# Optimization experiments

Measured on AMD Instinct MI355X. Metric: run time of the kernel, lower is better.

## Reference

```python
import jax, jax.numpy as jnp
from jax import lax
import numpy as np

NPOINT = 1024
NSAMPLE = 32
BN_EPS = 1e-3  # Keras BatchNormalization default epsilon


def farthest_point_sample(xyz, npoint):
    # xyz: [B, N, 3] -> indices [B, npoint] (int32), sequential O(npoint*N)
    B, N, _ = xyz.shape

    def step(carry, _):
        distance, farthest = carry                                   # [B,N], [B]
        centroid = jnp.take_along_axis(xyz, farthest[:, None, None], axis=1)  # [B,1,3]
        dist = jnp.sum((xyz - centroid) ** 2, axis=-1)               # [B,N]
        distance = jnp.minimum(distance, dist)
        new_farthest = jnp.argmax(distance, axis=1).astype(jnp.int32)
        return (distance, new_farthest), farthest

    init = (jnp.full((B, N), 1e10, xyz.dtype), jnp.zeros((B,), jnp.int32))
    _, idxs = lax.scan(step, init, xs=None, length=npoint)           # [npoint, B]
    return jnp.transpose(idxs)                                       # [B, npoint]


def index_points_2d(points, idx):
    # points: [B,N,C], idx: [B,S] -> [B,S,C]
    return jnp.take_along_axis(points, idx[:, :, None], axis=1)


def index_points_3d(points, idx):
    # points: [B,N,C], idx: [B,S,K] -> [B,S,K,C]
    return jax.vmap(lambda p, i: p[i])(points, idx)


def query_ball_point(nsample, xyz, new_xyz):
    # nearest-nsample variant (radius is ignored, matching the source)
    # sq_dist: [B, S, N]
    sq = jnp.sum(new_xyz ** 2, axis=-1, keepdims=True) \
         - 2.0 * jnp.einsum('bsc,bnc->bsn', new_xyz, xyz) \
         + jnp.sum(xyz ** 2, axis=-1)[:, None, :]
    _, group_idx = lax.top_k(-sq, nsample)                           # [B,S,K]
    return group_idx


def bn_relu(x, g, b, mm, mv):
    # inference-mode BatchNorm (moving stats) + ReLU, per-channel on last dim
    return jax.nn.relu((x - mm) * lax.rsqrt(mv + BN_EPS) * g + b)


def setup_inputs() -> dict:
    key = jax.random.key(0)
    ks = jax.random.split(key, 20)
    B, N, D = 4, 16384, 64
    mlp = [64, 64, 128]
    cin = 3 + D  # 67
    inp = {
        'xyz': jax.random.normal(ks[0], (B, N, 3), jnp.float32),
        'points': jax.random.normal(ks[1], (B, N, D), jnp.float32),
    }
    c = cin
    for i, co in enumerate(mlp):
        inp[f'w{i}'] = jax.random.normal(ks[2 + 4 * i], (c, co), jnp.float32) * (1.0 / np.sqrt(c))
        inp[f'g{i}'] = jnp.ones((co,), jnp.float32)
        inp[f'b{i}'] = jnp.zeros((co,), jnp.float32)
        inp[f'mm{i}'] = jax.random.normal(ks[3 + 4 * i], (co,), jnp.float32) * 0.1
        inp[f'mv{i}'] = jax.random.uniform(ks[4 + 4 * i], (co,), jnp.float32, 0.5, 1.5)
        c = co
    return inp


def reference(xyz, points, w0, g0, b0, mm0, mv0, w1, g1, b1, mm1, mv1, w2, g2, b2, mm2, mv2):
    fps_idx = farthest_point_sample(xyz, NPOINT)                     # [B,S]
    new_xyz = index_points_2d(xyz, fps_idx)                          # [B,S,3]
    idx = query_ball_point(NSAMPLE, xyz, new_xyz)                    # [B,S,K]
    grouped_xyz = index_points_3d(xyz, idx)                          # [B,S,K,3]
    grouped_xyz_norm = grouped_xyz - new_xyz[:, :, None, :]
    grouped_points = index_points_3d(points, idx)                    # [B,S,K,D]
    x = jnp.concatenate([grouped_xyz_norm, grouped_points], axis=-1) # [B,S,K,3+D]
    for w, g, b, mm, mv in ((w0, g0, b0, mm0, mv0), (w1, g1, b1, mm1, mv1), (w2, g2, b2, mm2, mv2)):
        x = bn_relu(jnp.einsum('bskc,co->bsko', x, w), g, b, mm, mv)
    new_points = jnp.max(x, axis=2)                                  # [B,S,C_out]
    return (new_xyz, new_points)
```

## Files before the change

### kernel.cpp

```cpp
#include <hip/hip_runtime.h>
#include <hip/hip_bf16.h>
#include <stdint.h>

#define N_PTS 16384
#define S_OUT 1024


typedef float v2f __attribute__((ext_vector_type(2)));

__global__ __launch_bounds__(512)
__attribute__((amdgpu_waves_per_eu(2, 2)))
void fps_kernel(
    const float* __restrict__ xyz,
    float* __restrict__ out_newxyz)
{
#pragma clang fp contract(off)
  const int b    = blockIdx.x;
  const int tid  = threadIdx.x;
  const int lane = tid & 63;
  const int wid  = tid >> 6;
  const float* base = xyz + (size_t)b * N_PTS * 3;

  v2f px[16], py[16], pz[16], dist[16];
#pragma unroll
  for (int i = 0; i < 16; ++i) {
    int n0 = (tid * 32 + 2 * i) * 3;
    px[i] = (v2f){ base[n0 + 0], base[n0 + 3] };
    py[i] = (v2f){ base[n0 + 1], base[n0 + 4] };
    pz[i] = (v2f){ base[n0 + 2], base[n0 + 5] };
    dist[i] = (v2f){ 1e10f, 1e10f };
  }

  __shared__ float swave[2][8];
  __shared__ unsigned s_idx[2];

  if (tid == 0) { s_idx[0] = 0xFFFFFFFFu; s_idx[1] = 0xFFFFFFFFu; }

  float cx = base[0], cy = base[1], cz = base[2];

  for (int s = 0; s < S_OUT; ++s) {
    if (tid == 0) {
      size_t o = ((size_t)b * S_OUT + s) * 3;
      out_newxyz[o + 0] = cx;
      out_newxyz[o + 1] = cy;
      out_newxyz[o + 2] = cz;
    }
    if (s == S_OUT - 1) break;

    const v2f cx2 = (v2f){ cx, cx };
    const v2f cy2 = (v2f){ cy, cy };
    const v2f cz2 = (v2f){ cz, cz };

    float m0 = -1.0f, m1 = -1.0f, m2 = -1.0f, m3 = -1.0f;
#pragma unroll
    for (int i = 0; i < 16; ++i) {
      v2f dx = px[i] - cx2;
      v2f dy = py[i] - cy2;
      v2f dz = pz[i] - cz2;
      v2f dd = (dx * dx + dy * dy) + dz * dz;
      v2f dm = __builtin_elementwise_min(dist[i], dd);
      dist[i] = dm;
      if ((i & 3) == 0)      m0 = fmaxf(fmaxf(m0, dm.x), dm.y);
      else if ((i & 3) == 1) m1 = fmaxf(fmaxf(m1, dm.x), dm.y);
      else if ((i & 3) == 2) m2 = fmaxf(fmaxf(m2, dm.x), dm.y);
      else                   m3 = fmaxf(fmaxf(m3, dm.x), dm.y);
    }
    const float lm = fmaxf(fmaxf(m0, m1), fmaxf(m2, m3));

    float wm = lm;
#pragma unroll
    for (int off = 1; off < 64; off <<= 1)
      wm = fmaxf(wm, __shfl_xor(wm, off));

    const int p = s & 1;
    if (lane == 0) swave[p][wid] = wm;
    __syncthreads();

    float M = swave[p][0];
    {
      float a = fmaxf(fmaxf(swave[p][1], swave[p][2]), swave[p][3]);
      float c = fmaxf(fmaxf(swave[p][4], swave[p][5]), swave[p][6]);
      M = fmaxf(fmaxf(M, swave[p][7]), fmaxf(a, c));
    }

    if (lm == M) {
      int bi = 0;
#pragma unroll
      for (int j = 31; j >= 0; --j) {
        float d = dist[j >> 1][j & 1];
        bi = (d == M) ? j : bi;
      }
      atomicMin(&s_idx[p], (unsigned)(tid * 32 + bi));
    }
    if (tid == 0) s_idx[p ^ 1] = 0xFFFFFFFFu;
    __syncthreads();

    unsigned n = s_idx[p];
    n = __builtin_amdgcn_readfirstlane(n);
    const float* pc = base + (size_t)n * 3;
    cx = pc[0]; cy = pc[1]; cz = pc[2];
  }
}

#define BBUF_CAP 1024

__global__ __launch_bounds__(256, 2) void knn_kernel(
    const float* __restrict__ xyz,
    const float* __restrict__ newxyz,
    int* __restrict__ knn_out)
{
  const int bs  = blockIdx.x;
  const int b   = bs >> 10;
  const int tid = threadIdx.x;
  const float* base = xyz + (size_t)b * N_PTS * 3;

  const float qx = newxyz[(size_t)bs * 3 + 0];
  const float qy = newxyz[(size_t)bs * 3 + 1];
  const float qz = newxyz[(size_t)bs * 3 + 2];
  const float sumq = __fadd_rn(__fadd_rn(__fmul_rn(qx, qx), __fmul_rn(qy, qy)),
                               __fmul_rn(qz, qz));

  __shared__ unsigned hist[2048];
  __shared__ unsigned tsum[256];
  __shared__ unsigned long long cand[512];
  __shared__ unsigned long long bbuf[BBUF_CAP];
  __shared__ unsigned long long s_min;
  __shared__ int s_b1, s_r1, s_b2, s_r2, s_cntL, s_cntC, s_cntB;

  for (int i = tid; i < 2048; i += 256) hist[i] = 0;
  if (tid == 0) { s_cntL = 0; s_cntC = 0; s_cntB = 0; }
  __syncthreads();

#define KNN_KEY(n, u)                                                          \
    float x = base[(n) * 3 + 0];                                               \
    float y = base[(n) * 3 + 1];                                               \
    float z = base[(n) * 3 + 2];                                               \
    float sumx = __fadd_rn(__fadd_rn(__fmul_rn(x, x), __fmul_rn(y, y)),        \
                           __fmul_rn(z, z));                                   \
    float dot  = __fmul_rn(qx, x);                                             \
    dot = fmaf(qy, y, dot);                                                    \
    dot = fmaf(qz, z, dot);                                                    \
    float sq   = __fsub_rn(__fadd_rn(sumq, sumx), __fmul_rn(2.0f, dot));       \
    unsigned u = __float_as_uint(sq);                                          \
    u ^= (u & 0x80000000u) ? 0xFFFFFFFFu : 0x80000000u;

  for (int j = 0; j < 64; ++j) {
    int n = j * 256 + tid;
    KNN_KEY(n, u)
    atomicAdd(&hist[u >> 21], 1u);
  }
  __syncthreads();

  unsigned ts = 0;
#pragma unroll
  for (int u = 0; u < 8; ++u) ts += hist[tid * 8 + u];
  tsum[tid] = ts;
  __syncthreads();

  if (tid == 0) {
    unsigned acc = 0; int t2 = 0;
    for (; t2 < 256; ++t2) { unsigned h = tsum[t2]; if (acc + h >= 32u) break; acc += h; }
    int u2 = t2 * 8;
    for (;; ++u2) { unsigned h = hist[u2]; if (acc + h >= 32u) break; acc += h; }
    s_b1 = u2; s_r1 = 32 - (int)acc;
  }
  __syncthreads();
  const unsigned b1 = (unsigned)s_b1;
  const int r1 = s_r1;

  for (int i = tid; i < 2048; i += 256) hist[i] = 0;
  __syncthreads();

  int* outp = knn_out + (size_t)bs * 32;

  for (int j = 0; j < 64; ++j) {
    int n = j * 256 + tid;
    KNN_KEY(n, u)
    unsigned bin = u >> 21;
    if (bin < b1) {
      int p = atomicAdd(&s_cntL, 1);
      outp[p] = n;
    } else if (bin == b1) {
      atomicAdd(&hist[(u >> 10) & 0x7FFu], 1u);
      int q = atomicAdd(&s_cntB, 1);
      if (q < BBUF_CAP)
        bbuf[q] = ((unsigned long long)u << 32) | (unsigned)n;
    }
  }
  __syncthreads();

  ts = 0;
#pragma unroll
  for (int u = 0; u < 8; ++u) ts += hist[tid * 8 + u];
  tsum[tid] = ts;
  __syncthreads();

  if (tid == 0) {
    unsigned acc = 0; int t2 = 0;
    for (; t2 < 256; ++t2) { unsigned h = tsum[t2]; if (acc + h >= (unsigned)r1) break; acc += h; }
    int u2 = t2 * 8;
    for (;; ++u2) { unsigned h = hist[u2]; if (acc + h >= (unsigned)r1) break; acc += h; }
    s_b2 = u2; s_r2 = r1 - (int)acc;
  }
  __syncthreads();
  const unsigned b2 = (unsigned)s_b2;
  const int cntB = s_cntB;

  if (cntB <= BBUF_CAP) {
    for (int q = tid; q < cntB; q += 256) {
      unsigned long long v = bbuf[q];
      unsigned u = (unsigned)(v >> 32);
      unsigned sub = (u >> 10) & 0x7FFu;
      if (sub < b2) {
        int p = atomicAdd(&s_cntL, 1);
        outp[p] = (int)(unsigned)(v & 0xFFFFFFFFull);
      } else if (sub == b2) {
        int p = atomicAdd(&s_cntC, 1);
        if (p < 512) cand[p] = v;
      }
    }
  } else {
    for (int j = 0; j < 64; ++j) {
      int n = j * 256 + tid;
      KNN_KEY(n, u)
      if ((u >> 21) == b1) {
        unsigned sub = (u >> 10) & 0x7FFu;
        if (sub < b2) {
          int p = atomicAdd(&s_cntL, 1);
          outp[p] = n;
        } else if (sub == b2) {
          int p = atomicAdd(&s_cntC, 1);
          if (p < 512) cand[p] = ((unsigned long long)u << 32) | (unsigned)n;
        }
      }
    }
  }
  __syncthreads();
#undef KNN_KEY

  const int r   = s_r2;
  const int cl  = s_cntL;
  const int cnt = min(s_cntC, 512);
  unsigned long long last = 0ull;
  for (int i = 0; i < r; ++i) {
    if (tid == 0) s_min = ~0ull;
    __syncthreads();
    for (int p = tid; p < cnt; p += 256) {
      unsigned long long v = cand[p];
      if (i == 0 ? 1 : (v > last)) atomicMin(&s_min, v);
    }
    __syncthreads();
    unsigned long long m = s_min;
    if (tid == 0) outp[cl + i] = (int)(unsigned)(m & 0xFFFFFFFFull);
    last = m;
    __syncthreads();
  }
}

__global__ __launch_bounds__(256, 2) void mlp_kernel(
    const float* __restrict__ xyz,
    const float* __restrict__ points,
    const float* __restrict__ newxyz,
    const int* __restrict__ knn,
    const float* __restrict__ w0, const float* __restrict__ g0,
    const float* __restrict__ b0, const float* __restrict__ mm0,
    const float* __restrict__ mv0,
    const float* __restrict__ w1, const float* __restrict__ g1,
    const float* __restrict__ b1_, const float* __restrict__ mm1,
    const float* __restrict__ mv1,
    const float* __restrict__ w2, const float* __restrict__ g2,
    const float* __restrict__ b2_, const float* __restrict__ mm2,
    const float* __restrict__ mv2,
    float* __restrict__ out1)
{
  const int tid = threadIdx.x;
  const int BS0 = blockIdx.x * 2;

  __shared__ __align__(16) float xT[2][67][36];
  __shared__ __align__(16) float a1[2][64][36];
  __shared__ __align__(16) float wbuf[8192];

  {
    const int sg = tid >> 7;
    const int j  = (tid >> 2) & 31;
    const int cq = tid & 3;
    const int S  = BS0 + sg;
    const int bb = S >> 10;
    const int n  = knn[(size_t)S * 32 + j] & (N_PTS - 1);
    const float* pbase = points + ((size_t)bb * N_PTS + n) * 64;
    const float* xbase = xyz + ((size_t)bb * N_PTS + n) * 3;
    for (int c = cq; c < 67; c += 4) {
      float v;
      if (c < 3) v = __fsub_rn(xbase[c], newxyz[(size_t)S * 3 + c]);
      else       v = pbase[c - 3];
      xT[sg][c][j] = v;
    }
  }
  for (int i = tid; i < 67 * 64; i += 256) wbuf[i] = w0[i];
  __syncthreads();

  const int sg = tid >> 7;
  const int t  = tid & 127;

  {
    const int ot = t & 15, kt = t >> 4;
    const int o0 = ot * 4, k0 = kt * 4;
    float acc[4][4] = {};
    for (int c = 0; c < 67; ++c) {
      float4 xv = *(const float4*)&xT[sg][c][k0];
      float4 wq = *(const float4*)&wbuf[c * 64 + o0];
      float wv[4] = { wq.x, wq.y, wq.z, wq.w };
      float xs[4] = { xv.x, xv.y, xv.z, xv.w };
#pragma unroll
      for (int a = 0; a < 4; ++a)
#pragma unroll
        for (int k2 = 0; k2 < 4; ++k2)
          acc[a][k2] = fmaf(wv[a], xs[k2], acc[a][k2]);
    }
#pragma unroll
    for (int jj = 0; jj < 4; ++jj) {
      int o = o0 + jj;
      float A  = rsqrtf(mv0[o] + 1e-3f) * g0[o];
      float Bc = b0[o] - mm0[o] * A;
      float4 y;
      y.x = fmaxf(fmaf(acc[jj][0], A, Bc), 0.0f);
      y.y = fmaxf(fmaf(acc[jj][1], A, Bc), 0.0f);
      y.z = fmaxf(fmaf(acc[jj][2], A, Bc), 0.0f);
      y.w = fmaxf(fmaf(acc[jj][3], A, Bc), 0.0f);
      *(float4*)&a1[sg][o][k0] = y;
    }
  }
  __syncthreads();
  for (int i = tid; i < 64 * 64; i += 256) wbuf[i] = w1[i];
  __syncthreads();

  {
    const int ot = t & 15, kt = t >> 4;
    const int o0 = ot * 4, k0 = kt * 4;
    float acc[4][4] = {};
    for (int c = 0; c < 64; ++c) {
      float4 xv = *(const float4*)&a1[sg][c][k0];
      float4 wq = *(const float4*)&wbuf[c * 64 + o0];
      float wv[4] = { wq.x, wq.y, wq.z, wq.w };
      float xs[4] = { xv.x, xv.y, xv.z, xv.w };
#pragma unroll
      for (int a = 0; a < 4; ++a)
#pragma unroll
        for (int k2 = 0; k2 < 4; ++k2)
          acc[a][k2] = fmaf(wv[a], xs[k2], acc[a][k2]);
    }
#pragma unroll
    for (int jj = 0; jj < 4; ++jj) {
      int o = o0 + jj;
      float A  = rsqrtf(mv1[o] + 1e-3f) * g1[o];
      float Bc = b1_[o] - mm1[o] * A;
      float4 y;
      y.x = fmaxf(fmaf(acc[jj][0], A, Bc), 0.0f);
      y.y = fmaxf(fmaf(acc[jj][1], A, Bc), 0.0f);
      y.z = fmaxf(fmaf(acc[jj][2], A, Bc), 0.0f);
      y.w = fmaxf(fmaf(acc[jj][3], A, Bc), 0.0f);
      *(float4*)&xT[sg][o][k0] = y;
    }
  }
  __syncthreads();
  for (int i = tid; i < 64 * 128; i += 256) wbuf[i] = w2[i];
  __syncthreads();

  float* pm = &a1[0][0][0];
  {
    const int ot = t & 31, kt = t >> 5;
    const int o0 = ot * 4, k0 = kt * 8;
    float acc[4][8] = {};
    for (int c = 0; c < 64; ++c) {
      float4 xa = *(const float4*)&xT[sg][c][k0];
      float4 xb = *(const float4*)&xT[sg][c][k0 + 4];
      float4 wq = *(const float4*)&wbuf[c * 128 + o0];
      float wv[4] = { wq.x, wq.y, wq.z, wq.w };
      float xs[8] = { xa.x, xa.y, xa.z, xa.w, xb.x, xb.y, xb.z, xb.w };
#pragma unroll
      for (int a = 0; a < 4; ++a)
#pragma unroll
        for (int k2 = 0; k2 < 8; ++k2)
          acc[a][k2] = fmaf(wv[a], xs[k2], acc[a][k2]);
    }
#pragma unroll
    for (int jj = 0; jj < 4; ++jj) {
      int o = o0 + jj;
      float A  = rsqrtf(mv2[o] + 1e-3f) * g2[o];
      float Bc = b2_[o] - mm2[o] * A;
      float m = 0.0f;
#pragma unroll
      for (int kk = 0; kk < 8; ++kk)
        m = fmaxf(m, fmaf(acc[jj][kk], A, Bc));
      pm[((sg * 128 + o) << 2) + kt] = m;
    }
  }
  __syncthreads();
  {
    const int sg2 = tid >> 7, o = tid & 127;
    const int basep = (sg2 * 128 + o) << 2;
    float m = fmaxf(fmaxf(pm[basep + 0], pm[basep + 1]),
                    fmaxf(pm[basep + 2], pm[basep + 3]));
    out1[(size_t)(BS0 + sg2) * 128 + o] = m;
  }
}

extern "C" void kernel_launch(void* const* d_in, const int* in_sizes, int n_in,
                              void* d_out, int out_size, void* d_ws, size_t ws_size,
                              hipStream_t stream) {
  const float* xyz    = (const float*)d_in[0];
  const float* points = (const float*)d_in[1];
  const float* w0  = (const float*)d_in[2];
  const float* g0  = (const float*)d_in[3];
  const float* b0  = (const float*)d_in[4];
  const float* mm0 = (const float*)d_in[5];
  const float* mv0 = (const float*)d_in[6];
  const float* w1  = (const float*)d_in[7];
  const float* g1  = (const float*)d_in[8];
  const float* b1  = (const float*)d_in[9];
  const float* mm1 = (const float*)d_in[10];
  const float* mv1 = (const float*)d_in[11];
  const float* w2  = (const float*)d_in[12];
  const float* g2  = (const float*)d_in[13];
  const float* b2  = (const float*)d_in[14];
  const float* mm2 = (const float*)d_in[15];
  const float* mv2 = (const float*)d_in[16];

  float* out      = (float*)d_out;
  float* out_pts  = out + (size_t)4 * 1024 * 3;
  int*   knn      = (int*)d_ws;

  fps_kernel<<<4, 512, 0, stream>>>(xyz, out);
  knn_kernel<<<4096, 256, 0, stream>>>(xyz, out, knn);
  mlp_kernel<<<2048, 256, 0, stream>>>(xyz, points, out, knn,
      w0, g0, b0, mm0, mv0, w1, g1, b1, mm1, mv1, w2, g2, b2, mm2, mv2,
      out_pts);
}
```

Before: 1.963 ms.

## Split farthest-point sampling across eight blocks per batch with global-memory reduction

Farthest-point sampling now uses 8 workgroups per batch instead of one, each holding 2048 points. Every iteration exchanges packed (distance, index) keys through global memory with release/acquire atomics and spin-waits on a sequence tag, which spreads the sequential argmax over more compute units. The in-block reduction also switches to a wave ballot plus a packed 64-bit key max, replacing the atomicMin scan. The cost is a cross-block global-memory round-trip on every one of the 1024 steps, a reliance on all 32 blocks being co-resident, and reuse of the knn workspace for the reduction slots.

```diff
diff --git a/kernel.cpp b/kernel.cpp
--- a/kernel.cpp
+++ b/kernel.cpp
@@ -8,38 +8,45 @@
 
 typedef float v2f __attribute__((ext_vector_type(2)));
 
-__global__ __launch_bounds__(512)
-__attribute__((amdgpu_waves_per_eu(2, 2)))
-void fps_kernel(
+__global__ __launch_bounds__(512) void fps_kernel(
     const float* __restrict__ xyz,
-    float* __restrict__ out_newxyz)
+    float* __restrict__ out_newxyz,
+    unsigned long long* __restrict__ g_red)
 {
 #pragma clang fp contract(off)
-  const int b    = blockIdx.x;
+  const int blk  = blockIdx.x;
+  const int b    = blk >> 3;
+  const int sub  = blk & 7;
   const int tid  = threadIdx.x;
   const int lane = tid & 63;
   const int wid  = tid >> 6;
   const float* base = xyz + (size_t)b * N_PTS * 3;
 
-  v2f px[16], py[16], pz[16], dist[16];
-#pragma unroll
-  for (int i = 0; i < 16; ++i) {
-    int n0 = (tid * 32 + 2 * i) * 3;
+  if (tid == 0) {
+    __hip_atomic_store(&g_red[b * 8 + sub], 0ull,
+                       __ATOMIC_RELEASE, __HIP_MEMORY_SCOPE_AGENT);
+    __hip_atomic_store(&g_red[32 + b * 8 + sub], 0ull,
+                       __ATOMIC_RELEASE, __HIP_MEMORY_SCOPE_AGENT);
+  }
+
+  const int p0 = sub * 2048 + tid * 4;
+  v2f px[2], py[2], pz[2], dist[2];
+#pragma unroll
+  for (int i = 0; i < 2; ++i) {
+    int n0 = (p0 + 2 * i) * 3;
     px[i] = (v2f){ base[n0 + 0], base[n0 + 3] };
     py[i] = (v2f){ base[n0 + 1], base[n0 + 4] };
     pz[i] = (v2f){ base[n0 + 2], base[n0 + 5] };
     dist[i] = (v2f){ 1e10f, 1e10f };
   }
 
-  __shared__ float swave[2][8];
-  __shared__ unsigned s_idx[2];
-
-  if (tid == 0) { s_idx[0] = 0xFFFFFFFFu; s_idx[1] = 0xFFFFFFFFu; }
+  __shared__ unsigned long long wkey[8];
+  __shared__ unsigned long long s_win;
 
   float cx = base[0], cy = base[1], cz = base[2];
 
   for (int s = 0; s < S_OUT; ++s) {
-    if (tid == 0) {
+    if (sub == 0 && tid == 0) {
       size_t o = ((size_t)b * S_OUT + s) * 3;
       out_newxyz[o + 0] = cx;
       out_newxyz[o + 1] = cy;
@@ -51,51 +58,64 @@
     const v2f cy2 = (v2f){ cy, cy };
     const v2f cz2 = (v2f){ cz, cz };
 
-    float m0 = -1.0f, m1 = -1.0f, m2 = -1.0f, m3 = -1.0f;
-#pragma unroll
-    for (int i = 0; i < 16; ++i) {
+    float best = -1.0f; int bj = 0;
+#pragma unroll
+    for (int i = 0; i < 2; ++i) {
       v2f dx = px[i] - cx2;
       v2f dy = py[i] - cy2;
       v2f dz = pz[i] - cz2;
       v2f dd = (dx * dx + dy * dy) + dz * dz;
       v2f dm = __builtin_elementwise_min(dist[i], dd);
       dist[i] = dm;
-      if ((i & 3) == 0)      m0 = fmaxf(fmaxf(m0, dm.x), dm.y);
-      else if ((i & 3) == 1) m1 = fmaxf(fmaxf(m1, dm.x), dm.y);
-      else if ((i & 3) == 2) m2 = fmaxf(fmaxf(m2, dm.x), dm.y);
-      else                   m3 = fmaxf(fmaxf(m3, dm.x), dm.y);
-    }
-    const float lm = fmaxf(fmaxf(m0, m1), fmaxf(m2, m3));
-
-    float wm = lm;
+      bool c0 = dm.x > best; best = c0 ? dm.x : best; bj = c0 ? (2 * i)     : bj;
+      bool c1 = dm.y > best; best = c1 ? dm.y : best; bj = c1 ? (2 * i + 1) : bj;
+    }
+    const unsigned bestN = (unsigned)(p0 + bj);
+
+    float wm = best;
 #pragma unroll
     for (int off = 1; off < 64; off <<= 1)
       wm = fmaxf(wm, __shfl_xor(wm, off));
-
-    const int p = s & 1;
-    if (lane == 0) swave[p][wid] = wm;
+    unsigned long long bal = __ballot(best == wm);
+    int wl = __ffsll(bal) - 1;
+    unsigned wn = (unsigned)__shfl((int)bestN, wl);
+
+    if (lane == 0)
+      wkey[wid] = ((unsigned long long)__float_as_uint(wm) << 32) |
+                  (unsigned long long)(0x3FFFu - wn);
     __syncthreads();
 
-    float M = swave[p][0];
-    {
-      float a = fmaxf(fmaxf(swave[p][1], swave[p][2]), swave[p][3]);
-      float c = fmaxf(fmaxf(swave[p][4], swave[p][5]), swave[p][6]);
-      M = fmaxf(fmaxf(M, swave[p][7]), fmaxf(a, c));
-    }
-
-    if (lm == M) {
-      int bi = 0;
-#pragma unroll
-      for (int j = 31; j >= 0; --j) {
-        float d = dist[j >> 1][j & 1];
-        bi = (d == M) ? j : bi;
+    if (wid == 0 && lane < 8) {
+      const unsigned want = (0x96u << 10) | (unsigned)(s + 1);
+      unsigned long long* slots = g_red + ((unsigned)(s + 1) & 1u) * 32 + b * 8;
+
+      unsigned long long k = wkey[lane];
+#pragma unroll
+      for (int off = 1; off < 8; off <<= 1) {
+        unsigned long long o = __shfl_xor(k, off);
+        if (o > k) k = o;
       }
-      atomicMin(&s_idx[p], (unsigned)(tid * 32 + bi));
-    }
-    if (tid == 0) s_idx[p ^ 1] = 0xFFFFFFFFu;
+      if (lane == 0)
+        __hip_atomic_store(&slots[sub],
+                           k | ((unsigned long long)want << 14),
+                           __ATOMIC_RELEASE, __HIP_MEMORY_SCOPE_AGENT);
+
+      unsigned long long v; int guard = 0;
+      do {
+        v = __hip_atomic_load(&slots[lane],
+                              __ATOMIC_ACQUIRE, __HIP_MEMORY_SCOPE_AGENT);
+      } while ((((unsigned)(v >> 14) & 0x3FFFFu) != want) &&
+               (++guard < (1 << 20)));
+#pragma unroll
+      for (int off = 1; off < 8; off <<= 1) {
+        unsigned long long o = __shfl_xor(v, off);
+        if (o > v) v = o;
+      }
+      if (lane == 0) s_win = v;
+    }
     __syncthreads();
 
-    unsigned n = s_idx[p];
+    unsigned n = 0x3FFFu - ((unsigned)s_win & 0x3FFFu);
     n = __builtin_amdgcn_readfirstlane(n);
     const float* pc = base + (size_t)n * 3;
     cx = pc[0]; cy = pc[1]; cz = pc[2];
@@ -429,8 +449,9 @@
   float* out      = (float*)d_out;
   float* out_pts  = out + (size_t)4 * 1024 * 3;
   int*   knn      = (int*)d_ws;
-
-  fps_kernel<<<4, 512, 0, stream>>>(xyz, out);
+  unsigned long long* g_red = (unsigned long long*)d_ws;
+
+  fps_kernel<<<32, 512, 0, stream>>>(xyz, out, g_red);
   knn_kernel<<<4096, 256, 0, stream>>>(xyz, out, knn);
   mlp_kernel<<<2048, 256, 0, stream>>>(xyz, points, out, knn,
       w0, g0, b0, mm0, mv0, w1, g1, b1, mm1, mv1, w2, g2, b2, mm2, mv2,
```

Result: slower. 2.342 ms (+19.3%).
